# Optimization experiments

Measured on AMD Instinct MI355X. Metric: run time of the kernel, lower is better.

Reference implementation:

```python
import jax, jax.numpy as jnp
import numpy as np

B, T = 2097152, 32
EPS = 1e-07


def setup_inputs() -> dict:
    key = jax.random.key(0)
    k1, k2, k3 = jax.random.split(key, 3)
    logits = jax.random.normal(k1, (B, T), dtype=jnp.float32)
    time_bins = jax.random.randint(k2, (B,), 0, T, dtype=jnp.int64)
    events = jax.random.randint(k3, (B,), 0, 2, dtype=jnp.int32)
    return {"logits": logits, "time_bins": time_bins, "events": events}


def reference(logits, time_bins, events):
    Bn, Tn = logits.shape
    hazards = jax.nn.sigmoid(logits)                      # [B, T]
    t = jnp.clip(time_bins, 0, Tn - 1).astype(jnp.int32)  # [B]
    # sum of log(1 - h) over bins strictly before t (masked, vectorized)
    before = jnp.arange(Tn, dtype=jnp.int32)[None, :] < t[:, None]  # [B, T]
    log_one_minus = jnp.log(1.0 - hazards + EPS)
    log_surv = jnp.sum(jnp.where(before, log_one_minus, 0.0), axis=1)  # [B]
    # hazard at the event/censoring bin
    h_t = jnp.take_along_axis(hazards, t[:, None], axis=1)[:, 0]       # [B]
    term = jnp.where(events == 1,
                     jnp.log(h_t + EPS),
                     jnp.log(1.0 - h_t + EPS))
    loss = -(log_surv + term)  # [B]
    return jnp.mean(loss)      # reduction='mean'
```

## Files before the change

kernel.cpp:

```cpp
#include <hip/hip_runtime.h>


constexpr int T_BINS        = 32;
constexpr int BLOCK         = 256;
constexpr int LANES_PER_ROW = 8;
constexpr int ROWS_PER_ITER = BLOCK / LANES_PER_ROW;
constexpr int NBLOCKS       = 2048;
constexpr int U             = 4;
constexpr int STEP          = U * ROWS_PER_ITER;
constexpr int PIPE          = 2 * STEP;

__device__ __forceinline__ int detect_shift(const int* tb, int lane) {
    const int probe = tb[2 * lane + 1];
    return (__ballot(probe != 0) == 0ULL) ? 1 : 0;
}

__device__ __forceinline__ void block_reduce_store(float acc, float* dst, int tid) {
    #pragma unroll
    for (int off = 32; off > 0; off >>= 1)
        acc += __shfl_down(acc, off, 64);
    __shared__ float sw[BLOCK / 64];
    if ((tid & 63) == 0) sw[tid >> 6] = acc;
    __syncthreads();
    if (tid == 0) *dst = sw[0] + sw[1] + sw[2] + sw[3];
}

__global__ __launch_bounds__(BLOCK) void dhl_main_fast(
    const float4* __restrict__ logits4,
    const int*    __restrict__ tb,
    const int*    __restrict__ ev,
    float*        __restrict__ partials,
    int rows_per_block)
{
    const int tid   = threadIdx.x;
    const int shift = detect_shift(tb, tid & 63);
    const int lane8 = tid & (LANES_PER_ROW - 1);
    const int rloc  = tid >> 3;
    const int j0    = lane8 * 4;
    const int rbase = blockIdx.x * rows_per_block;

    float4 vA[U]; int tA[U]; int eA[U];
    float4 vB[U]; int tB[U]; int eB[U];
    float acc = 0.0f;

#define DHL_LOAD(V, T, E, base)                                                 \
    _Pragma("unroll")                                                           \
    for (int u = 0; u < U; ++u) {                                               \
        const int row_ = (base) + u * ROWS_PER_ITER + rloc;                     \
        V[u] = logits4[row_ * LANES_PER_ROW + lane8];                           \
        T[u] = tb[row_ << shift];                                               \
        E[u] = ev[row_];                                                        \
    }

#define DHL_COMPUTE(V, T, E)                                                    \
    _Pragma("unroll")                                                           \
    for (int u = 0; u < U; ++u) {                                               \
        const int tt_ = min(max(T[u], 0), T_BINS - 1);                          \
        const float xs_[4] = {V[u].x, V[u].y, V[u].z, V[u].w};                  \
        _Pragma("unroll")                                                       \
        for (int c = 0; c < 4; ++c) {                                           \
            const float x_ = xs_[c];                                            \
            const float L_ = __logf(1.0f + __expf(x_));                         \
            const int j_ = j0 + c;                                              \
            if (j_ <= tt_) acc -= L_;                                           \
            if (j_ == tt_ && E[u] == 1) acc += x_;                              \
        }                                                                       \
    }

    DHL_LOAD(vA, tA, eA, rbase)
    for (int i = 0; i < rows_per_block; i += PIPE) {
        DHL_LOAD(vB, tB, eB, rbase + i + STEP)
        DHL_COMPUTE(vA, tA, eA)
        if (i + PIPE < rows_per_block) {
            DHL_LOAD(vA, tA, eA, rbase + i + PIPE)
        }
        DHL_COMPUTE(vB, tB, eB)
    }
#undef DHL_LOAD
#undef DHL_COMPUTE

    block_reduce_store(acc, &partials[blockIdx.x], tid);
}

__global__ __launch_bounds__(BLOCK) void dhl_main_safe(
    const float4* __restrict__ logits4,
    const int*    __restrict__ tb,
    const int*    __restrict__ ev,
    float*        __restrict__ partials,
    long long nrows, int rows_per_block)
{
    const int tid   = threadIdx.x;
    const int shift = detect_shift(tb, tid & 63);
    const int lane8 = tid & (LANES_PER_ROW - 1);
    const int rloc  = tid >> 3;
    const int j0    = lane8 * 4;
    const long long rbase = (long long)blockIdx.x * rows_per_block;

    float acc = 0.0f;
    for (int i = 0; i < rows_per_block; i += ROWS_PER_ITER) {
        const long long row = rbase + i + rloc;
        if (row < nrows) {
            const float4 v = logits4[row * LANES_PER_ROW + lane8];
            int t = tb[row << shift];
            t = min(max(t, 0), T_BINS - 1);
            const int e = ev[row];
            const float xs[4] = {v.x, v.y, v.z, v.w};
            #pragma unroll
            for (int c = 0; c < 4; ++c) {
                const float x = xs[c];
                const float L = __logf(1.0f + __expf(x));
                const int j = j0 + c;
                if (j <= t) acc -= L;
                if (j == t && e == 1) acc += x;
            }
        }
    }
    block_reduce_store(acc, &partials[blockIdx.x], tid);
}

__global__ __launch_bounds__(BLOCK) void dhl_finalize(
    const float* __restrict__ partials, int n, float* __restrict__ out, float scale)
{
    const int tid = threadIdx.x;
    float acc = 0.0f;
    for (int i = tid; i < n; i += BLOCK) acc += partials[i];
    #pragma unroll
    for (int off = 32; off > 0; off >>= 1)
        acc += __shfl_down(acc, off, 64);
    __shared__ float sw[BLOCK / 64];
    if ((tid & 63) == 0) sw[tid >> 6] = acc;
    __syncthreads();
    if (tid == 0)
        out[0] = (sw[0] + sw[1] + sw[2] + sw[3]) * scale;
}

extern "C" void kernel_launch(void* const* d_in, const int* in_sizes, int n_in,
                              void* d_out, int out_size, void* d_ws, size_t ws_size,
                              hipStream_t stream) {
    const float4* logits4 = (const float4*)d_in[0];
    const int*    tb      = (const int*)d_in[1];
    const int*    ev      = (const int*)d_in[2];
    float*        out     = (float*)d_out;
    const int B = in_sizes[1];

    float* partials = (float*)d_ws;

    int rows_per_block = (B + NBLOCKS - 1) / NBLOCKS;
    rows_per_block = ((rows_per_block + PIPE - 1) / PIPE) * PIPE;
    const int nblocks = (B + rows_per_block - 1) / rows_per_block;

    const bool fast = (B % rows_per_block == 0) && (B <= (1 << 27));
    if (fast) {
        dhl_main_fast<<<nblocks, BLOCK, 0, stream>>>(logits4, tb, ev, partials, rows_per_block);
    } else {
        dhl_main_safe<<<nblocks, BLOCK, 0, stream>>>(logits4, tb, ev, partials,
                                                     (long long)B, rows_per_block);
    }
    dhl_finalize<<<1, BLOCK, 0, stream>>>(partials, nblocks, out, -1.0f / (float)B);
}
```

Measured before the change: 53.94 us.

## Skip loading logits past each row's time bin via staged time-bin prefetch

Time bins are now loaded three steps ahead in a 4-deep ring, so the logits load for each row can be redirected to an already-fetched lane's address when that lane's columns are all beyond the row's bin. Redundant addresses in the same cache lines are meant to reduce DRAM traffic for the roughly half of logits that never contribute. The pipeline is restructured into a 3-stage software pipeline, and the row chunk rounding changes to 4*STEP. The trade is more registers and more index arithmetic. The loads still issue, so the saving only comes from cache-line coalescing of the redirected addresses.

```diff
diff --git a/kernel.cpp b/kernel.cpp
--- a/kernel.cpp
+++ b/kernel.cpp
@@ -8,7 +8,7 @@
 constexpr int NBLOCKS       = 2048;
 constexpr int U             = 4;
 constexpr int STEP          = U * ROWS_PER_ITER;
-constexpr int PIPE          = 2 * STEP;
+constexpr int CHUNK         = 4 * STEP;
 
 __device__ __forceinline__ int detect_shift(const int* tb, int lane) {
     const int probe = tb[2 * lane + 1];
@@ -38,46 +38,65 @@
     const int rloc  = tid >> 3;
     const int j0    = lane8 * 4;
     const int rbase = blockIdx.x * rows_per_block;
+    const int nb    = rows_per_block / STEP;
 
-    float4 vA[U]; int tA[U]; int eA[U];
-    float4 vB[U]; int tB[U]; int eB[U];
-    float acc = 0.0f;
+    int    tq[4][U];
+    float4 vq[2][U];
+    int    eq[2][U];
+    float  acc = 0.0f;
 
-#define DHL_LOAD(V, T, E, base)                                                 \
+#define DHL_LOADT(Td, b)                                                        \
     _Pragma("unroll")                                                           \
     for (int u = 0; u < U; ++u) {                                               \
-        const int row_ = (base) + u * ROWS_PER_ITER + rloc;                     \
-        V[u] = logits4[row_ * LANES_PER_ROW + lane8];                           \
-        T[u] = tb[row_ << shift];                                               \
-        E[u] = ev[row_];                                                        \
+        const int row_ = rbase + (b) * STEP + u * ROWS_PER_ITER + rloc;         \
+        Td[u] = min(max(tb[row_ << shift], 0), T_BINS - 1);                     \
     }
 
-#define DHL_COMPUTE(V, T, E)                                                    \
+#define DHL_LOADVE(Vd, Ed, Ts, b)                                               \
     _Pragma("unroll")                                                           \
     for (int u = 0; u < U; ++u) {                                               \
-        const int tt_ = min(max(T[u], 0), T_BINS - 1);                          \
-        const float xs_[4] = {V[u].x, V[u].y, V[u].z, V[u].w};                  \
+        const int row_ = rbase + (b) * STEP + u * ROWS_PER_ITER + rloc;         \
+        const int col_ = (j0 <= Ts[u]) ? lane8 : (lane8 & 3);                   \
+        Vd[u] = logits4[row_ * LANES_PER_ROW + col_];                           \
+        Ed[u] = ev[row_];                                                       \
+    }
+
+#define DHL_COMPUTE(Vs, Ts, Es)                                                 \
+    _Pragma("unroll")                                                           \
+    for (int u = 0; u < U; ++u) {                                               \
+        const int tt_ = Ts[u];                                                  \
+        const float xs_[4] = {Vs[u].x, Vs[u].y, Vs[u].z, Vs[u].w};              \
         _Pragma("unroll")                                                       \
         for (int c = 0; c < 4; ++c) {                                           \
             const float x_ = xs_[c];                                            \
             const float L_ = __logf(1.0f + __expf(x_));                         \
             const int j_ = j0 + c;                                              \
             if (j_ <= tt_) acc -= L_;                                           \
-            if (j_ == tt_ && E[u] == 1) acc += x_;                              \
+            if (j_ == tt_ && Es[u] == 1) acc += x_;                             \
         }                                                                       \
     }
 
-    DHL_LOAD(vA, tA, eA, rbase)
-    for (int i = 0; i < rows_per_block; i += PIPE) {
-        DHL_LOAD(vB, tB, eB, rbase + i + STEP)
-        DHL_COMPUTE(vA, tA, eA)
-        if (i + PIPE < rows_per_block) {
-            DHL_LOAD(vA, tA, eA, rbase + i + PIPE)
-        }
-        DHL_COMPUTE(vB, tB, eB)
+#define DHL_STEP(jj)                                                            \
+    DHL_LOADT(tq[((jj) + 3) & 3], min(b4 + (jj) + 3, nb - 1))                   \
+    DHL_LOADVE(vq[((jj) + 1) & 1], eq[((jj) + 1) & 1], tq[((jj) + 1) & 3],      \
+               min(b4 + (jj) + 1, nb - 1))                                      \
+    DHL_COMPUTE(vq[(jj) & 1], tq[(jj) & 3], eq[(jj) & 1])
+
+    DHL_LOADT(tq[0], 0)
+    DHL_LOADT(tq[1], 1)
+    DHL_LOADT(tq[2], 2)
+    DHL_LOADVE(vq[0], eq[0], tq[0], 0)
+
+    for (int b4 = 0; b4 < nb; b4 += 4) {
+        DHL_STEP(0)
+        DHL_STEP(1)
+        DHL_STEP(2)
+        DHL_STEP(3)
     }
-#undef DHL_LOAD
+#undef DHL_STEP
 #undef DHL_COMPUTE
+#undef DHL_LOADVE
+#undef DHL_LOADT
 
     block_reduce_store(acc, &partials[blockIdx.x], tid);
 }
@@ -146,7 +165,7 @@
     float* partials = (float*)d_ws;
 
     int rows_per_block = (B + NBLOCKS - 1) / NBLOCKS;
-    rows_per_block = ((rows_per_block + PIPE - 1) / PIPE) * PIPE;
+    rows_per_block = ((rows_per_block + CHUNK - 1) / CHUNK) * CHUNK;
     const int nblocks = (B + rows_per_block - 1) / rows_per_block;
 
     const bool fast = (B % rows_per_block == 0) && (B <= (1 << 27));
```

Measured after the change: 55.68 us. 3.2% more time.
